# Kernel optimization log

Measured on AMD Instinct MI355X. Metric: run time of the kernel, lower is better.

The kernel has to match this reference:

```python
import jax, jax.numpy as jnp
import numpy as np

N = 100_000   # nodes
E = 3_200_000 # directed edges
EC = 16       # edge_channels

def setup_inputs() -> dict:
    key = jax.random.key(0)
    ks = jax.random.split(key, 9)
    x = jax.random.normal(ks[0], (N, 8), jnp.float32)
    adjs = jax.random.randint(ks[1], (2, E), 0, N, jnp.int32)
    edge_attr = jax.random.normal(ks[2], (E, EC), jnp.float32)
    s = 1.0 / np.sqrt(EC)
    lin_e_w = jax.random.uniform(ks[3], (1, EC), jnp.float32, -s, s)
    lin_e_b = jax.random.uniform(ks[4], (1,), jnp.float32, -s, s)
    aggr2_w = jax.random.uniform(ks[5], (1, 4), jnp.float32, -0.5, 0.5)
    aggr2_b = jax.random.uniform(ks[6], (1,), jnp.float32, -0.5, 0.5)
    lin_l_w = jax.random.uniform(ks[7], (1, 1), jnp.float32, -1.0, 1.0)
    lin_l_b = jax.random.uniform(ks[8], (1,), jnp.float32, -1.0, 1.0)
    return dict(x=x, adjs=adjs, edge_attr=edge_attr,
                lin_e_w=lin_e_w, lin_e_b=lin_e_b,
                aggr2_w=aggr2_w, aggr2_b=aggr2_b,
                lin_l_w=lin_l_w, lin_l_b=lin_l_b)

def reference(x, adjs, edge_attr, lin_e_w, lin_e_b, aggr2_w, aggr2_b, lin_l_w, lin_l_b):
    n = x.shape[0]
    # layer 0 (EdgeConv): edge MLP edge_channels -> 1
    ev = (edge_attr @ lin_e_w.T + lin_e_b)[:, 0]            # [E]
    src, dst = adjs[0], adjs[1]
    # to_undirected: edges + reversed edges; row 1 (scatter dest) = cat(dst, src)
    u_idx = jnp.concatenate([dst, src])                      # [2E]
    u_val = jnp.concatenate([ev, ev])                        # [2E]
    cnt = jax.ops.segment_sum(jnp.ones_like(u_val), u_idx, num_segments=n)
    nsum = jax.ops.segment_sum(u_val, u_idx, num_segments=n)
    nmax = jnp.where(cnt > 0, jax.ops.segment_max(u_val, u_idx, num_segments=n), 0.0)
    nmin = jnp.where(cnt > 0, jax.ops.segment_min(u_val, u_idx, num_segments=n), 0.0)
    nmean = nsum / jnp.maximum(cnt, 1.0)                     # torch-scatter mean: 0 for empty

    def inv_clean(node_vals):
        r = 1.0 / node_vals[dst]                             # propagate -> x_i = x[edge_index[1]]
        return jnp.where(jnp.isnan(r) | (r == jnp.inf), 1.0, r)

    nc = jnp.stack([inv_clean(nmax), inv_clean(nmean), inv_clean(nmin), inv_clean(nsum)], axis=1)  # [E,4]
    ec = jnp.where(jnp.isnan(ev) | (ev == jnp.inf), 1.0, ev)[:, None]   # cleaned edge_attr [E,1]
    nc2 = nc @ aggr2_w.T + aggr2_b                            # [E,1]
    out = (ec @ lin_l_w.T + lin_l_b) + nc2 * ec               # [E,1]
    out = jnp.where(out == jnp.inf, 1.0, out)
    return out.reshape(-1)                                    # torch.flatten
```

## Files before the change

kernel.cpp:

```cpp
#include <hip/hip_runtime.h>

#define INF_F (__builtin_inff())
#define PMAX 512
#define G1 512
#define NPART 256


__device__ __forceinline__ unsigned int enc_f(float f) {
    unsigned int u = __float_as_uint(f);
    return (u & 0x80000000u) ? ~u : (u | 0x80000000u);
}
__device__ __forceinline__ float dec_f(unsigned int u) {
    unsigned int b = (u & 0x80000000u) ? (u & 0x7FFFFFFFu) : ~u;
    return __uint_as_float(b);
}
__device__ __forceinline__ float inv_clean(float x) {
    float r = 1.0f / x;
    if (isnan(r) || r == INF_F) r = 1.0f;
    return r;
}
__device__ __forceinline__ float edge_final(float ev, float c, float lw, float lb) {
    float ec = (isnan(ev) || ev == INF_F) ? 1.0f : ev;
    float out = ec * lw + lb + c * ec;
    if (out == INF_F) out = 1.0f;
    return out;
}
__device__ __forceinline__ float dot16_bias(const float* __restrict__ edge_attr,
                                            const float* __restrict__ lin_e_w,
                                            const float* __restrict__ lin_e_b, int e) {
    const float4* ea = reinterpret_cast<const float4*>(edge_attr) + (size_t)e * 4;
    const float4* w4 = reinterpret_cast<const float4*>(lin_e_w);
    float4 a0 = ea[0], a1 = ea[1], a2 = ea[2], a3 = ea[3];
    float4 w0 = w4[0], w1 = w4[1], w2 = w4[2], w3 = w4[3];
    return a0.x * w0.x + a0.y * w0.y + a0.z * w0.z + a0.w * w0.w
         + a1.x * w1.x + a1.y * w1.y + a1.z * w1.z + a1.w * w1.w
         + a2.x * w2.x + a2.y * w2.y + a2.z * w2.z + a2.w * w2.w
         + a3.x * w3.x + a3.y * w3.y + a3.z * w3.z + a3.w * w3.w
         + lin_e_b[0];
}


__global__ void __launch_bounds__(256)
k1_ev_count(const float* __restrict__ edge_attr,
            const int* __restrict__ src, const int* __restrict__ dst,
            const float* __restrict__ lin_e_w, const float* __restrict__ lin_e_b,
            float* __restrict__ ev_out, unsigned int* __restrict__ gh,
            int E, int P, int CE) {
    __shared__ unsigned int hist[PMAX];
    int t = threadIdx.x, b = blockIdx.x;
    for (int p = t; p < P; p += 256) hist[p] = 0u;
    __syncthreads();
    int start = b * CE, end = min(E, start + CE);
    for (int e = start + t; e < end; e += 256) {
        float ev = dot16_bias(edge_attr, lin_e_w, lin_e_b, e);
        ev_out[e] = ev;
        atomicAdd(&hist[(unsigned int)src[e] >> 8], 1u);
        atomicAdd(&hist[(unsigned int)dst[e] >> 8], 1u);
    }
    __syncthreads();
    for (int p = t; p < P; p += 256) gh[(size_t)b * P + p] = hist[p];
}

__global__ void __launch_bounds__(256)
k2_scan_cols(unsigned int* __restrict__ gh, unsigned int* __restrict__ ptotal, int P) {
    int p = blockIdx.x, t = threadIdx.x;
    unsigned int v0 = gh[(size_t)(2 * t) * P + p];
    unsigned int v1 = gh[(size_t)(2 * t + 1) * P + p];
    unsigned int s = v0 + v1;
    __shared__ unsigned int sc[256];
    sc[t] = s;
    __syncthreads();
    for (int off = 1; off < 256; off <<= 1) {
        unsigned int x = (t >= off) ? sc[t - off] : 0u;
        __syncthreads();
        sc[t] += x;
        __syncthreads();
    }
    unsigned int run = sc[t] - s;
    gh[(size_t)(2 * t) * P + p] = run;
    gh[(size_t)(2 * t + 1) * P + p] = run + v0;
    if (t == 255) ptotal[p] = run + v0 + v1;
}

__global__ void k3_scan_part(const unsigned int* __restrict__ ptotal,
                             unsigned int* __restrict__ pbase, int P) {
    int t = threadIdx.x;
    unsigned int u0 = (2 * t < P) ? ptotal[2 * t] : 0u;
    unsigned int u1 = (2 * t + 1 < P) ? ptotal[2 * t + 1] : 0u;
    unsigned int s = u0 + u1;
    __shared__ unsigned int sc[256];
    sc[t] = s;
    __syncthreads();
    for (int off = 1; off < 256; off <<= 1) {
        unsigned int x = (t >= off) ? sc[t - off] : 0u;
        __syncthreads();
        sc[t] += x;
        __syncthreads();
    }
    unsigned int excl = sc[t] - s;
    if (2 * t < P) pbase[2 * t] = excl;
    if (2 * t + 1 < P) pbase[2 * t + 1] = excl + u0;
}

__global__ void __launch_bounds__(256)
k4_scatter(const int* __restrict__ src, const int* __restrict__ dst,
           const float* __restrict__ ev_in,
           const unsigned int* __restrict__ gh, const unsigned int* __restrict__ pbase,
           uint2* __restrict__ rec, int E, int P, int CE) {
    __shared__ unsigned int cur[PMAX];
    int t = threadIdx.x, b = blockIdx.x;
    for (int p = t; p < P; p += 256) cur[p] = pbase[p] + gh[(size_t)b * P + p];
    __syncthreads();
    int start = b * CE, end = min(E, start + CE);
    for (int e = start + t; e < end; e += 256) {
        float ev = ev_in[e];
        unsigned int ebits = __float_as_uint(ev);
        unsigned int s = (unsigned int)src[e], d = (unsigned int)dst[e];
        unsigned int pos = atomicAdd(&cur[d >> 8], 1u);
        rec[pos] = make_uint2(ebits, d & 255u);
        pos = atomicAdd(&cur[s >> 8], 1u);
        rec[pos] = make_uint2(ebits, s & 255u);
    }
}

__global__ void __launch_bounds__(256)
k5_reduce(const uint2* __restrict__ rec,
          const unsigned int* __restrict__ gh, const unsigned int* __restrict__ pbase,
          const unsigned int* __restrict__ ptotal,
          const float* __restrict__ aggr2_w, const float* __restrict__ aggr2_b,
          float* __restrict__ nodeC, int N, int P) {
    __shared__ float ssum[NPART];
    __shared__ unsigned int scnt[NPART], smax[NPART], smin[NPART];
    int p = blockIdx.x, t = threadIdx.x;
    ssum[t] = 0.0f; scnt[t] = 0u; smax[t] = 0u; smin[t] = 0xFFFFFFFFu;
    __syncthreads();
    unsigned int pb = pbase[p], ptot = ptotal[p];
    for (int b = t; b < G1; b += 256) {
        unsigned int o0 = gh[(size_t)b * P + p];
        unsigned int o1 = (b + 1 < G1) ? gh[(size_t)(b + 1) * P + p] : ptot;
        const uint2* r = rec + pb + o0;
        unsigned int c = o1 - o0;
        for (unsigned int i = 0; i < c; ++i) {
            uint2 q = r[i];
            float v = __uint_as_float(q.x);
            unsigned int l = q.y;
            unsigned int eu = enc_f(v);
            atomicAdd(&ssum[l], v);
            atomicAdd(&scnt[l], 1u);
            atomicMax(&smax[l], eu);
            atomicMin(&smin[l], eu);
        }
    }
    __syncthreads();
    int node = p * NPART + t;
    if (node < N) {
        unsigned int c = scnt[t];
        float sum = ssum[t];
        float mxv = (c > 0u) ? dec_f(smax[t]) : 0.0f;
        float mnv = (c > 0u) ? dec_f(smin[t]) : 0.0f;
        float mean = sum / fmaxf((float)c, 1.0f);
        float4 w = *reinterpret_cast<const float4*>(aggr2_w);
        nodeC[node] = w.x * inv_clean(mxv) + w.y * inv_clean(mean)
                    + w.z * inv_clean(mnv) + w.w * inv_clean(sum) + aggr2_b[0];
    }
}

__global__ void __launch_bounds__(256)
edge_out(float* __restrict__ evout, const int* __restrict__ dst,
         const float* __restrict__ nodeC,
         const float* __restrict__ lin_l_w, const float* __restrict__ lin_l_b,
         int E) {
    int i = blockIdx.x * blockDim.x + threadIdx.x;
    int base = i * 4;
    float lw = lin_l_w[0], lb = lin_l_b[0];
    if (base + 3 < E) {
        float4 ev = *reinterpret_cast<const float4*>(evout + base);
        int4 d = *reinterpret_cast<const int4*>(dst + base);
        float4 o;
        o.x = edge_final(ev.x, nodeC[d.x], lw, lb);
        o.y = edge_final(ev.y, nodeC[d.y], lw, lb);
        o.z = edge_final(ev.z, nodeC[d.z], lw, lb);
        o.w = edge_final(ev.w, nodeC[d.w], lw, lb);
        *reinterpret_cast<float4*>(evout + base) = o;
    } else {
        for (int e = base; e < E; ++e)
            evout[e] = edge_final(evout[e], nodeC[dst[e]], lw, lb);
    }
}


__global__ void init_nodes_fb(unsigned long long* __restrict__ sc,
                              unsigned int* __restrict__ mx,
                              unsigned int* __restrict__ mn, int total) {
    int i = blockIdx.x * blockDim.x + threadIdx.x;
    if (i < total) { sc[i] = 0ull; mx[i] = 0u; mn[i] = 0xFFFFFFFFu; }
}

__global__ void __launch_bounds__(256)
edge_scatter_fb(const float* __restrict__ edge_attr,
                const int* __restrict__ src, const int* __restrict__ dst,
                const float* __restrict__ lin_e_w, const float* __restrict__ lin_e_b,
                float* __restrict__ ev_out,
                unsigned long long* __restrict__ sc,
                unsigned int* __restrict__ mx, unsigned int* __restrict__ mn,
                int E, int N, int repMask) {
    int e = blockIdx.x * blockDim.x + threadIdx.x;
    if (e >= E) return;
    float ev = dot16_bias(edge_attr, lin_e_w, lin_e_b, e);
    ev_out[e] = ev;
    unsigned long long packed =
        (1ull << 52) | (unsigned long long)((ev + 32.0f) * 1048576.0f);
    unsigned int u = enc_f(ev);
    int base = (blockIdx.x & repMask) * N;
    int s = src[e] + base, d = dst[e] + base;
    atomicAdd(&sc[d], packed);
    atomicAdd(&sc[s], packed);
    atomicMax(&mx[d], u);
    atomicMax(&mx[s], u);
    atomicMin(&mn[d], u);
    atomicMin(&mn[s], u);
}

__global__ void node_combine_fb(const unsigned long long* __restrict__ sc,
                                const unsigned int* __restrict__ mx,
                                const unsigned int* __restrict__ mn,
                                const float* __restrict__ aggr2_w,
                                const float* __restrict__ aggr2_b,
                                float* __restrict__ nodeC, int n, int R) {
    int v = blockIdx.x * blockDim.x + threadIdx.x;
    if (v >= n) return;
    unsigned long long acc = 0ull;
    unsigned int M = 0u, m = 0xFFFFFFFFu;
    for (int r = 0; r < R; ++r) {
        acc += sc[(size_t)r * n + v];
        M = max(M, mx[(size_t)r * n + v]);
        m = min(m, mn[(size_t)r * n + v]);
    }
    unsigned long long icnt = acc >> 52;
    float cnt = (float)icnt;
    double sumfix = (double)(acc & ((1ull << 52) - 1ull));
    float sum = (float)(sumfix * (1.0 / 1048576.0) - 32.0 * (double)icnt);
    float mxv, mnv;
    if (icnt > 0) { mxv = dec_f(M); mnv = dec_f(m); }
    else          { mxv = 0.0f;     mnv = 0.0f; }
    float mean = sum / fmaxf(cnt, 1.0f);
    float4 w = *reinterpret_cast<const float4*>(aggr2_w);
    nodeC[v] = w.x * inv_clean(mxv) + w.y * inv_clean(mean)
             + w.z * inv_clean(mnv) + w.w * inv_clean(sum) + aggr2_b[0];
}

static inline size_t align16(size_t x) { return (x + 15) & ~(size_t)15; }

extern "C" void kernel_launch(void* const* d_in, const int* in_sizes, int n_in,
                              void* d_out, int out_size, void* d_ws, size_t ws_size,
                              hipStream_t stream) {
    const int N = in_sizes[0] / 8;
    const int E = in_sizes[1] / 2;

    const int*   adjs      = (const int*)d_in[1];
    const int*   src       = adjs;
    const int*   dst       = adjs + E;
    const float* edge_attr = (const float*)d_in[2];
    const float* lin_e_w   = (const float*)d_in[3];
    const float* lin_e_b   = (const float*)d_in[4];
    const float* aggr2_w   = (const float*)d_in[5];
    const float* aggr2_b   = (const float*)d_in[6];
    const float* lin_l_w   = (const float*)d_in[7];
    const float* lin_l_b   = (const float*)d_in[8];
    float* out = (float*)d_out;

    const int B = 256;
    char* ws = (char*)d_ws;

    const int P = (N + NPART - 1) / NPART;
    const int CE = (E + G1 - 1) / G1;

    size_t off_gh = 0;
    size_t off_pt = align16(off_gh + (size_t)G1 * P * 4);
    size_t off_pb = align16(off_pt + (size_t)PMAX * 4);
    size_t off_rc = align16(off_pb + (size_t)PMAX * 4);
    size_t off_nc = align16(off_rc + (size_t)2 * E * 8);
    size_t need_sort = off_nc + (size_t)N * 4;

    if (P <= PMAX && (P & 1) == 0 + P <= PMAX && ws_size >= need_sort) {  }

    if (P <= PMAX && ws_size >= need_sort) {
        unsigned int* gh     = (unsigned int*)(ws + off_gh);
        unsigned int* ptotal = (unsigned int*)(ws + off_pt);
        unsigned int* pbase  = (unsigned int*)(ws + off_pb);
        uint2*        rec    = (uint2*)(ws + off_rc);
        float*        nodeC  = (float*)(ws + off_nc);

        hipLaunchKernelGGL(k1_ev_count, dim3(G1), dim3(B), 0, stream,
                           edge_attr, src, dst, lin_e_w, lin_e_b, out, gh, E, P, CE);
        hipLaunchKernelGGL(k2_scan_cols, dim3(P), dim3(B), 0, stream, gh, ptotal, P);
        hipLaunchKernelGGL(k3_scan_part, dim3(1), dim3(B), 0, stream, ptotal, pbase, P);
        hipLaunchKernelGGL(k4_scatter, dim3(G1), dim3(B), 0, stream,
                           src, dst, out, gh, pbase, rec, E, P, CE);
        hipLaunchKernelGGL(k5_reduce, dim3(P), dim3(B), 0, stream,
                           rec, gh, pbase, ptotal, aggr2_w, aggr2_b, nodeC, N, P);
        int nt = (E + 3) / 4;
        hipLaunchKernelGGL(edge_out, dim3((nt + B - 1) / B), dim3(B), 0, stream,
                           out, dst, nodeC, lin_l_w, lin_l_b, E);
    } else {
        int R = 8;
        while (R > 1 && (size_t)R * N * 16 + (size_t)N * 4 > ws_size) R >>= 1;
        unsigned long long* sc    = (unsigned long long*)ws;
        unsigned int*       mx    = (unsigned int*)(sc + (size_t)R * N);
        unsigned int*       mn    = mx + (size_t)R * N;
        float*              nodeC = (float*)(mn + (size_t)R * N);

        int totalRN = R * N;
        hipLaunchKernelGGL(init_nodes_fb, dim3((totalRN + B - 1) / B), dim3(B), 0, stream,
                           sc, mx, mn, totalRN);
        hipLaunchKernelGGL(edge_scatter_fb, dim3((E + B - 1) / B), dim3(B), 0, stream,
                           edge_attr, src, dst, lin_e_w, lin_e_b,
                           out, sc, mx, mn, E, N, R - 1);
        hipLaunchKernelGGL(node_combine_fb, dim3((N + B - 1) / B), dim3(B), 0, stream,
                           sc, mx, mn, aggr2_w, aggr2_b, nodeC, N, R);
        int nt = (E + 3) / 4;
        hipLaunchKernelGGL(edge_out, dim3((nt + B - 1) / B), dim3(B), 0, stream,
                           out, dst, nodeC, lin_l_w, lin_l_b, E);
    }
}
```

Measured before the change: 177.9 us.

## Pad per-block bucket segments to multiples of eight and stream records flat in reduce

The scan now rounds each block's per-partition count up to a multiple of eight, so every block segment in the record buffer is aligned. The scatter kernel fills the unused padding slots with marker records. The reduce kernel then reads the whole partition range as coalesced 16-byte loads across all threads and skips marker entries, instead of each thread walking one block's segment serially. This removes the uncoalesced, load-imbalanced per-segment loops, at the cost of extra padding writes, a larger record buffer and marker checks.

```diff
diff --git a/kernel.cpp b/kernel.cpp
--- a/kernel.cpp
+++ b/kernel.cpp
@@ -4,6 +4,7 @@
 #define PMAX 512
 #define G1 512
 #define NPART 256
+#define MARKER 0xFFFFFFFFu
 
 
 __device__ __forceinline__ unsigned int enc_f(float f) {
@@ -64,8 +65,8 @@
 __global__ void __launch_bounds__(256)
 k2_scan_cols(unsigned int* __restrict__ gh, unsigned int* __restrict__ ptotal, int P) {
     int p = blockIdx.x, t = threadIdx.x;
-    unsigned int v0 = gh[(size_t)(2 * t) * P + p];
-    unsigned int v1 = gh[(size_t)(2 * t + 1) * P + p];
+    unsigned int v0 = (gh[(size_t)(2 * t) * P + p] + 7u) & ~7u;
+    unsigned int v1 = (gh[(size_t)(2 * t + 1) * P + p] + 7u) & ~7u;
     unsigned int s = v0 + v1;
     __shared__ unsigned int sc[256];
     sc[t] = s;
@@ -106,6 +107,7 @@
 k4_scatter(const int* __restrict__ src, const int* __restrict__ dst,
            const float* __restrict__ ev_in,
            const unsigned int* __restrict__ gh, const unsigned int* __restrict__ pbase,
+           const unsigned int* __restrict__ ptotal,
            uint2* __restrict__ rec, int E, int P, int CE) {
     __shared__ unsigned int cur[PMAX];
     int t = threadIdx.x, b = blockIdx.x;
@@ -121,34 +123,45 @@
         pos = atomicAdd(&cur[s >> 8], 1u);
         rec[pos] = make_uint2(ebits, s & 255u);
     }
+    __syncthreads();
+    for (int p = t; p < P; p += 256) {
+        unsigned int rend = pbase[p] +
+            ((b + 1 < G1) ? gh[(size_t)(b + 1) * P + p] : ptotal[p]);
+        for (unsigned int q = cur[p]; q < rend; ++q)
+            rec[q] = make_uint2(0u, MARKER);
+    }
 }
 
 __global__ void __launch_bounds__(256)
 k5_reduce(const uint2* __restrict__ rec,
-          const unsigned int* __restrict__ gh, const unsigned int* __restrict__ pbase,
-          const unsigned int* __restrict__ ptotal,
+          const unsigned int* __restrict__ pbase, const unsigned int* __restrict__ ptotal,
           const float* __restrict__ aggr2_w, const float* __restrict__ aggr2_b,
-          float* __restrict__ nodeC, int N, int P) {
+          float* __restrict__ nodeC, int N) {
     __shared__ float ssum[NPART];
     __shared__ unsigned int scnt[NPART], smax[NPART], smin[NPART];
     int p = blockIdx.x, t = threadIdx.x;
     ssum[t] = 0.0f; scnt[t] = 0u; smax[t] = 0u; smin[t] = 0xFFFFFFFFu;
     __syncthreads();
-    unsigned int pb = pbase[p], ptot = ptotal[p];
-    for (int b = t; b < G1; b += 256) {
-        unsigned int o0 = gh[(size_t)b * P + p];
-        unsigned int o1 = (b + 1 < G1) ? gh[(size_t)(b + 1) * P + p] : ptot;
-        const uint2* r = rec + pb + o0;
-        unsigned int c = o1 - o0;
-        for (unsigned int i = 0; i < c; ++i) {
-            uint2 q = r[i];
+    unsigned int pb = pbase[p], tot = ptotal[p];
+    const uint4* r4 = reinterpret_cast<const uint4*>(rec + pb);
+    unsigned int n4 = tot >> 1;
+    for (unsigned int i = t; i < n4; i += 256) {
+        uint4 q = r4[i];
+        if (q.y != MARKER) {
             float v = __uint_as_float(q.x);
-            unsigned int l = q.y;
             unsigned int eu = enc_f(v);
-            atomicAdd(&ssum[l], v);
-            atomicAdd(&scnt[l], 1u);
-            atomicMax(&smax[l], eu);
-            atomicMin(&smin[l], eu);
+            atomicAdd(&ssum[q.y], v);
+            atomicAdd(&scnt[q.y], 1u);
+            atomicMax(&smax[q.y], eu);
+            atomicMin(&smin[q.y], eu);
+        }
+        if (q.w != MARKER) {
+            float v = __uint_as_float(q.z);
+            unsigned int eu = enc_f(v);
+            atomicAdd(&ssum[q.w], v);
+            atomicAdd(&scnt[q.w], 1u);
+            atomicMax(&smax[q.w], eu);
+            atomicMin(&smin[q.w], eu);
         }
     }
     __syncthreads();
@@ -249,7 +262,7 @@
              + w.z * inv_clean(mnv) + w.w * inv_clean(sum) + aggr2_b[0];
 }
 
-static inline size_t align16(size_t x) { return (x + 15) & ~(size_t)15; }
+static inline size_t align64(size_t x) { return (x + 63) & ~(size_t)63; }
 
 extern "C" void kernel_launch(void* const* d_in, const int* in_sizes, int n_in,
                               void* d_out, int out_size, void* d_ws, size_t ws_size,
@@ -275,14 +288,13 @@
     const int P = (N + NPART - 1) / NPART;
     const int CE = (E + G1 - 1) / G1;
 
+    size_t max_rec = (size_t)2 * E + (size_t)G1 * P * 8;
     size_t off_gh = 0;
-    size_t off_pt = align16(off_gh + (size_t)G1 * P * 4);
-    size_t off_pb = align16(off_pt + (size_t)PMAX * 4);
-    size_t off_rc = align16(off_pb + (size_t)PMAX * 4);
-    size_t off_nc = align16(off_rc + (size_t)2 * E * 8);
+    size_t off_pt = align64(off_gh + (size_t)G1 * P * 4);
+    size_t off_pb = align64(off_pt + (size_t)PMAX * 4);
+    size_t off_rc = align64(off_pb + (size_t)PMAX * 4);
+    size_t off_nc = align64(off_rc + max_rec * 8);
     size_t need_sort = off_nc + (size_t)N * 4;
-
-    if (P <= PMAX && (P & 1) == 0 + P <= PMAX && ws_size >= need_sort) {  }
 
     if (P <= PMAX && ws_size >= need_sort) {
         unsigned int* gh     = (unsigned int*)(ws + off_gh);
@@ -296,9 +308,9 @@
         hipLaunchKernelGGL(k2_scan_cols, dim3(P), dim3(B), 0, stream, gh, ptotal, P);
         hipLaunchKernelGGL(k3_scan_part, dim3(1), dim3(B), 0, stream, ptotal, pbase, P);
         hipLaunchKernelGGL(k4_scatter, dim3(G1), dim3(B), 0, stream,
-                           src, dst, out, gh, pbase, rec, E, P, CE);
+                           src, dst, out, gh, pbase, ptotal, rec, E, P, CE);
         hipLaunchKernelGGL(k5_reduce, dim3(P), dim3(B), 0, stream,
-                           rec, gh, pbase, ptotal, aggr2_w, aggr2_b, nodeC, N, P);
+                           rec, pbase, ptotal, aggr2_w, aggr2_b, nodeC, N);
         int nt = (E + 3) / 4;
         hipLaunchKernelGGL(edge_out, dim3((nt + B - 1) / B), dim3(B), 0, stream,
                            out, dst, nodeC, lin_l_w, lin_l_b, E);
```

After: 174.8 us. No clear change (-1.7%).
